# Optimization experiments

Measured on AMD Instinct MI355X. Metric: run time of the kernel, lower is better.

The kernel has to match this reference:

```python
import jax, jax.numpy as jnp
import numpy as np

H = 2048   # hidden_size
SW = 256   # stack_width
SD = 200   # stack_depth
V = 128    # input_size (vocab)
O = 128    # output_size


def setup_inputs() -> dict:
    key = jax.random.key(0)
    ks = jax.random.split(key, 14)
    s = 0.02
    return {
        'inp': jax.random.randint(ks[0], (1,), 0, V),
        'hidden': jax.random.normal(ks[1], (1, 1, H), jnp.float32),
        'stack': jax.random.normal(ks[2], (1, SD, SW), jnp.float32),
        'emb': jax.random.normal(ks[3], (V, H), jnp.float32) * s,
        'Wc': jax.random.normal(ks[4], (3, H), jnp.float32) * s,
        'bc': jax.random.normal(ks[5], (3,), jnp.float32) * s,
        'Ws': jax.random.normal(ks[6], (SW, H), jnp.float32) * s,
        'bs': jax.random.normal(ks[7], (SW,), jnp.float32) * s,
        'W_ih': jax.random.normal(ks[8], (3 * H, H + SW), jnp.float32) * s,
        'b_ih': jax.random.normal(ks[9], (3 * H,), jnp.float32) * s,
        'W_hh': jax.random.normal(ks[10], (3 * H, H), jnp.float32) * s,
        'b_hh': jax.random.normal(ks[11], (3 * H,), jnp.float32) * s,
        'Wd': jax.random.normal(ks[12], (O, H), jnp.float32) * s,
        'bd': jax.random.normal(ks[13], (O,), jnp.float32) * s,
    }


def reference(inp, hidden, stack, emb, Wc, bc, Ws, bs, W_ih, b_ih, W_hh, b_hh, Wd, bd):
    # embedding: inp.view(1,-1) -> (1,1) -> (1,1,H)
    x = emb[inp.reshape(1, -1)]
    # stack controls: softmax(Linear(hidden.squeeze(0)))  -> (1,3)
    ctrl = jax.nn.softmax(hidden[0] @ Wc.T + bc, axis=1)
    # stack input: tanh(Linear(hidden)) -> (1,1,SW); permute(1,0,2) is identity for (1,1,SW)
    s_in = jnp.tanh(hidden @ Ws.T + bs)
    s_in = jnp.transpose(s_in, (1, 0, 2))  # (batch=1, 1, SW)
    # differentiable stack push/pop/no-op
    B, _, W = stack.shape
    a_push = ctrl[:, 0][:, None, None]
    a_pop = ctrl[:, 1][:, None, None]
    a_noop = ctrl[:, 2][:, None, None]
    zeros_bot = jnp.zeros((B, 1, W), dtype=stack.dtype)
    stack_down = jnp.concatenate([stack[:, 1:], zeros_bot], axis=1)
    stack_up = jnp.concatenate([s_in, stack[:, :-1]], axis=1)
    new_stack = a_noop * stack + a_push * stack_up + a_pop * stack_down
    stack_top = new_stack[:, 0, :][None]  # (1,1,SW)
    # single-step GRU (PyTorch gate order: r, z, n)
    gin = jnp.concatenate([x, stack_top], axis=2).reshape(1, -1)  # (1, H+SW)
    h = hidden.reshape(1, -1)                                      # (1, H)
    gi = gin @ W_ih.T + b_ih
    gh = h @ W_hh.T + b_hh
    r = jax.nn.sigmoid(gi[:, :H] + gh[:, :H])
    z = jax.nn.sigmoid(gi[:, H:2 * H] + gh[:, H:2 * H])
    n = jnp.tanh(gi[:, 2 * H:] + r * gh[:, 2 * H:])
    h_new = (1.0 - z) * n + z * h
    out = h_new @ Wd.T + bd  # (1, O)
    return out, h_new[None], new_stack
```

## Files before the change

kernel.cpp:

```cpp
#include <hip/hip_runtime.h>
#include <math.h>

#define H   2048
#define SW  256
#define SD  200
#define GIN (H + SW)
#define G3H (3 * H)
#define OO  128

#define STOP_OFF 8
#define GI_OFF   512
#define GH_OFF   (GI_OFF + G3H)

__device__ __forceinline__ float wave_reduce(float v) {
#pragma unroll
    for (int off = 32; off > 0; off >>= 1)
        v += __shfl_down(v, off, 64);
    return v;
}

__device__ __forceinline__ float sigmoidf(float x) {
    return 1.f / (1.f + expf(-x));
}

__device__ __forceinline__ float dot4(float4 a, float4 b) {
    return a.x * b.x + a.y * b.y + a.z * b.z + a.w * b.w;
}

__global__ __launch_bounds__(256) void k_stack(
        const float* __restrict__ hidden,
        const float* __restrict__ stack,
        const float* __restrict__ Wc,
        const float* __restrict__ bc,
        const float* __restrict__ Ws,
        const float* __restrict__ bs,
        float* __restrict__ ws,
        float* __restrict__ out_stack ) {
    __shared__ float sc[3];
    int tid = threadIdx.x;
    if (tid < 64) {
        float c0 = 0.f, c1 = 0.f, c2 = 0.f;
        for (int k = tid; k < H; k += 64) {
            float hv = hidden[k];
            c0 += hv * Wc[k];
            c1 += hv * Wc[H + k];
            c2 += hv * Wc[2 * H + k];
        }
        c0 = wave_reduce(c0); c1 = wave_reduce(c1); c2 = wave_reduce(c2);
        if (tid == 0) {
            c0 += bc[0]; c1 += bc[1]; c2 += bc[2];
            float m = fmaxf(c0, fmaxf(c1, c2));
            float e0 = expf(c0 - m), e1 = expf(c1 - m), e2 = expf(c2 - m);
            float inv = 1.f / (e0 + e1 + e2);
            sc[0] = e0 * inv;
            sc[1] = e1 * inv;
            sc[2] = e2 * inv;
        }
    }
    __syncthreads();
    float a_push = sc[0], a_pop = sc[1], a_noop = sc[2];
    int b = blockIdx.x;
    if (b < 64) {
        int wave = tid >> 6, lane = tid & 63;
        int row = b * 4 + wave;
        const float4* h4 = (const float4*)hidden;
        const float4* w4 = (const float4*)(Ws + row * H);
        float sum = 0.f;
#pragma unroll
        for (int i = 0; i < 8; ++i) {
            float4 a = h4[lane + i * 64];
            float4 c = w4[lane + i * 64];
            sum += dot4(a, c);
        }
        sum = wave_reduce(sum);
        if (lane == 0) {
            float s = tanhf(sum + bs[row]);
            float top = a_noop * stack[row] + a_push * s + a_pop * stack[SW + row];
            ws[STOP_OFF + row] = top;
            out_stack[row] = top;
        }
    } else {
        int rbase = 1 + (b - 64) * 4;
#pragma unroll
        for (int r = 0; r < 4; ++r) {
            int row = rbase + r;
            if (row >= SD) break;
            int idx = row * SW + tid;
            float dn = (row < SD - 1) ? stack[idx + SW] : 0.f;
            out_stack[idx] = a_noop * stack[idx] + a_push * stack[idx - SW] + a_pop * dn;
        }
    }
}

__global__ __launch_bounds__(256) void k_gemv(
        const float* __restrict__ hidden,
        const float* __restrict__ emb,
        const int* __restrict__ inp,
        const float* __restrict__ W_ih, const float* __restrict__ b_ih,
        const float* __restrict__ W_hh, const float* __restrict__ b_hh,
        float* __restrict__ ws) {
    __shared__ __align__(16) float vec[GIN];
    int b = blockIdx.x;
    int tid = threadIdx.x;
    bool is_gi = (b < 384);
    if (is_gi) {
        int e = inp[0];
        const float* er = emb + (long)e * H;
        for (int k = tid; k < H; k += 256) vec[k] = er[k];
        for (int k = H + tid; k < GIN; k += 256) vec[k] = ws[STOP_OFF + (k - H)];
    } else {
        for (int k = tid; k < H; k += 256) vec[k] = hidden[k];
    }
    __syncthreads();
    int wave = tid >> 6, lane = tid & 63;
    int rbase = (is_gi ? b : b - 384) * 16 + wave * 4;
    const float* W    = is_gi ? W_ih : W_hh;
    const float* bias = is_gi ? b_ih : b_hh;
    int K  = is_gi ? GIN : H;
    int K4 = K >> 2;
    const float4* v4 = (const float4*)vec;
    const float4* w0 = (const float4*)(W + (long)(rbase + 0) * K);
    const float4* w1 = (const float4*)(W + (long)(rbase + 1) * K);
    const float4* w2 = (const float4*)(W + (long)(rbase + 2) * K);
    const float4* w3 = (const float4*)(W + (long)(rbase + 3) * K);
    float s0 = 0.f, s1 = 0.f, s2 = 0.f, s3 = 0.f;
    int i = lane;
    for (; i + 64 < K4; i += 128) {
        int j = i + 64;
        float4 a0  = v4[i],  a1  = v4[j];
        float4 b00 = w0[i],  b01 = w0[j];
        float4 b10 = w1[i],  b11 = w1[j];
        float4 b20 = w2[i],  b21 = w2[j];
        float4 b30 = w3[i],  b31 = w3[j];
        s0 += dot4(a0, b00) + dot4(a1, b01);
        s1 += dot4(a0, b10) + dot4(a1, b11);
        s2 += dot4(a0, b20) + dot4(a1, b21);
        s3 += dot4(a0, b30) + dot4(a1, b31);
    }
    if (i < K4) {
        float4 a0 = v4[i];
        s0 += dot4(a0, w0[i]);
        s1 += dot4(a0, w1[i]);
        s2 += dot4(a0, w2[i]);
        s3 += dot4(a0, w3[i]);
    }
    s0 = wave_reduce(s0);
    s1 = wave_reduce(s1);
    s2 = wave_reduce(s2);
    s3 = wave_reduce(s3);
    float* dst = ws + (is_gi ? GI_OFF : GH_OFF);
    if (lane == 0) {
        dst[rbase + 0] = s0 + bias[rbase + 0];
        dst[rbase + 1] = s1 + bias[rbase + 1];
        dst[rbase + 2] = s2 + bias[rbase + 2];
        dst[rbase + 3] = s3 + bias[rbase + 3];
    }
}

__global__ __launch_bounds__(256) void k_out(
        const float* __restrict__ hidden,
        const float* __restrict__ Wd, const float* __restrict__ bd,
        const float* __restrict__ ws,
        float* __restrict__ d_out) {
    __shared__ __align__(16) float hn[H];
    int tid = threadIdx.x;
    const float* gi = ws + GI_OFF;
    const float* gh = ws + GH_OFF;
    for (int i = tid; i < H; i += 256) {
        float r = sigmoidf(gi[i] + gh[i]);
        float z = sigmoidf(gi[H + i] + gh[H + i]);
        float n = tanhf(gi[2 * H + i] + r * gh[2 * H + i]);
        float v = (1.f - z) * n + z * hidden[i];
        hn[i] = v;
        if (blockIdx.x == 0) d_out[OO + i] = v;
    }
    __syncthreads();
    int wave = tid >> 6, lane = tid & 63;
    int row = blockIdx.x * 4 + wave;
    const float4* h4 = (const float4*)hn;
    const float4* w4 = (const float4*)(Wd + (long)row * H);
    float sum = 0.f;
#pragma unroll
    for (int i = 0; i < 8; ++i) {
        float4 a = h4[lane + i * 64];
        float4 c = w4[lane + i * 64];
        sum += dot4(a, c);
    }
    sum = wave_reduce(sum);
    if (lane == 0) d_out[row] = sum + bd[row];
}

extern "C" void kernel_launch(void* const* d_in, const int* in_sizes, int n_in,
                              void* d_out, int out_size, void* d_ws, size_t ws_size,
                              hipStream_t stream) {
    const int*   inp    = (const int*)d_in[0];
    const float* hidden = (const float*)d_in[1];
    const float* stack  = (const float*)d_in[2];
    const float* emb    = (const float*)d_in[3];
    const float* Wc     = (const float*)d_in[4];
    const float* bc     = (const float*)d_in[5];
    const float* Ws     = (const float*)d_in[6];
    const float* bs     = (const float*)d_in[7];
    const float* W_ih   = (const float*)d_in[8];
    const float* b_ih   = (const float*)d_in[9];
    const float* W_hh   = (const float*)d_in[10];
    const float* b_hh   = (const float*)d_in[11];
    const float* Wd     = (const float*)d_in[12];
    const float* bd     = (const float*)d_in[13];
    float* out = (float*)d_out;
    float* ws  = (float*)d_ws;

    k_stack<<<114, 256, 0, stream>>>(hidden, stack, Wc, bc, Ws, bs, ws, out + OO + H);
    k_gemv<<<768, 256, 0, stream>>>(hidden, emb, inp, W_ih, b_ih, W_hh, b_hh, ws);
    k_out<<<32, 256, 0, stream>>>(hidden, Wd, bd, ws, out);
}
```

Before: 179.6 us.

## Fuse three kernels into one with atomic-counter inter-block dependencies

Replaces the three sequential launches (stack update, GI/GH GEMVs, GRU+output) with one fused kernel whose blocks wait on global atomic counters. GI blocks compute the embedding portion of their dot product before spinning on the stack-top counter, which overlaps the bulk of the W_ih read with the stack computation. Output blocks spin until all GEMV blocks have signalled. This removes launch gaps and kernel boundaries, at the cost of an extra memset launch and a deadlock risk if the spinning blocks become resident before the producer blocks they wait on.

Result: slower. 330.6 us (+84.1%).

```diff
diff --git a/kernel.cpp b/kernel.cpp
--- a/kernel.cpp
+++ b/kernel.cpp
@@ -12,6 +12,17 @@
 #define GI_OFF   512
 #define GH_OFF   (GI_OFF + G3H)
 
+#define NB_SIN  64
+#define NB_ELEM 50
+#define NB_GH   384
+#define NB_GI   384
+#define NB_OUT  32
+#define B_ELEM  NB_SIN
+#define B_GH    (B_ELEM + NB_ELEM)
+#define B_GI    (B_GH + NB_GH)
+#define B_OUT   (B_GI + NB_GI)
+#define NBLK    (B_OUT + NB_OUT)
+
 __device__ __forceinline__ float wave_reduce(float v) {
 #pragma unroll
     for (int off = 32; off > 0; off >>= 1)
@@ -27,167 +38,178 @@
     return a.x * b.x + a.y * b.y + a.z * b.z + a.w * b.w;
 }
 
-__global__ __launch_bounds__(256) void k_stack(
+__device__ __forceinline__ unsigned ld_acq(const unsigned* p) {
+    return __hip_atomic_load(p, __ATOMIC_ACQUIRE, __HIP_MEMORY_SCOPE_AGENT);
+}
+
+__device__ __forceinline__ void signal_done(unsigned* c) {
+    __threadfence();
+    __hip_atomic_fetch_add(c, 1u, __ATOMIC_RELEASE, __HIP_MEMORY_SCOPE_AGENT);
+}
+
+__global__ __launch_bounds__(256, 4) void k_fused(
         const float* __restrict__ hidden,
         const float* __restrict__ stack,
-        const float* __restrict__ Wc,
-        const float* __restrict__ bc,
-        const float* __restrict__ Ws,
-        const float* __restrict__ bs,
-        float* __restrict__ ws,
-        float* __restrict__ out_stack ) {
-    __shared__ float sc[3];
-    int tid = threadIdx.x;
-    if (tid < 64) {
-        float c0 = 0.f, c1 = 0.f, c2 = 0.f;
-        for (int k = tid; k < H; k += 64) {
-            float hv = hidden[k];
-            c0 += hv * Wc[k];
-            c1 += hv * Wc[H + k];
-            c2 += hv * Wc[2 * H + k];
-        }
-        c0 = wave_reduce(c0); c1 = wave_reduce(c1); c2 = wave_reduce(c2);
-        if (tid == 0) {
-            c0 += bc[0]; c1 += bc[1]; c2 += bc[2];
-            float m = fmaxf(c0, fmaxf(c1, c2));
-            float e0 = expf(c0 - m), e1 = expf(c1 - m), e2 = expf(c2 - m);
-            float inv = 1.f / (e0 + e1 + e2);
-            sc[0] = e0 * inv;
-            sc[1] = e1 * inv;
-            sc[2] = e2 * inv;
-        }
-    }
-    __syncthreads();
-    float a_push = sc[0], a_pop = sc[1], a_noop = sc[2];
-    int b = blockIdx.x;
-    if (b < 64) {
-        int wave = tid >> 6, lane = tid & 63;
-        int row = b * 4 + wave;
-        const float4* h4 = (const float4*)hidden;
-        const float4* w4 = (const float4*)(Ws + row * H);
-        float sum = 0.f;
-#pragma unroll
-        for (int i = 0; i < 8; ++i) {
-            float4 a = h4[lane + i * 64];
-            float4 c = w4[lane + i * 64];
-            sum += dot4(a, c);
-        }
-        sum = wave_reduce(sum);
-        if (lane == 0) {
-            float s = tanhf(sum + bs[row]);
-            float top = a_noop * stack[row] + a_push * s + a_pop * stack[SW + row];
-            ws[STOP_OFF + row] = top;
-            out_stack[row] = top;
-        }
-    } else {
-        int rbase = 1 + (b - 64) * 4;
-#pragma unroll
-        for (int r = 0; r < 4; ++r) {
-            int row = rbase + r;
-            if (row >= SD) break;
-            int idx = row * SW + tid;
-            float dn = (row < SD - 1) ? stack[idx + SW] : 0.f;
-            out_stack[idx] = a_noop * stack[idx] + a_push * stack[idx - SW] + a_pop * dn;
-        }
-    }
-}
-
-__global__ __launch_bounds__(256) void k_gemv(
-        const float* __restrict__ hidden,
         const float* __restrict__ emb,
-        const int* __restrict__ inp,
+        const int*   __restrict__ inp,
+        const float* __restrict__ Wc, const float* __restrict__ bc,
+        const float* __restrict__ Ws, const float* __restrict__ bs,
         const float* __restrict__ W_ih, const float* __restrict__ b_ih,
         const float* __restrict__ W_hh, const float* __restrict__ b_hh,
-        float* __restrict__ ws) {
-    __shared__ __align__(16) float vec[GIN];
+        const float* __restrict__ Wd, const float* __restrict__ bd,
+        float* __restrict__ ws,
+        float* __restrict__ d_out) {
+    __shared__ __align__(16) float lds[H];
+    unsigned* ctr = (unsigned*)ws;
+    float* out_stack = d_out + OO + H;
     int b = blockIdx.x;
     int tid = threadIdx.x;
-    bool is_gi = (b < 384);
-    if (is_gi) {
-        int e = inp[0];
-        const float* er = emb + (long)e * H;
-        for (int k = tid; k < H; k += 256) vec[k] = er[k];
-        for (int k = H + tid; k < GIN; k += 256) vec[k] = ws[STOP_OFF + (k - H)];
-    } else {
-        for (int k = tid; k < H; k += 256) vec[k] = hidden[k];
+    int wave = tid >> 6, lane = tid & 63;
+
+    if (b < B_GH) {
+        if (tid < 64) {
+            float c0 = 0.f, c1 = 0.f, c2 = 0.f;
+            for (int k = tid; k < H; k += 64) {
+                float hv = hidden[k];
+                c0 += hv * Wc[k];
+                c1 += hv * Wc[H + k];
+                c2 += hv * Wc[2 * H + k];
+            }
+            c0 = wave_reduce(c0); c1 = wave_reduce(c1); c2 = wave_reduce(c2);
+            if (tid == 0) {
+                c0 += bc[0]; c1 += bc[1]; c2 += bc[2];
+                float m = fmaxf(c0, fmaxf(c1, c2));
+                float e0 = expf(c0 - m), e1 = expf(c1 - m), e2 = expf(c2 - m);
+                float inv = 1.f / (e0 + e1 + e2);
+                lds[0] = e0 * inv;
+                lds[1] = e1 * inv;
+                lds[2] = e2 * inv;
+            }
+        }
+        __syncthreads();
+        float a_push = lds[0], a_pop = lds[1], a_noop = lds[2];
+        if (b < B_ELEM) {
+            int row = b * 4 + wave;
+            const float4* h4 = (const float4*)hidden;
+            const float4* w4 = (const float4*)(Ws + row * H);
+            float sum = 0.f;
+#pragma unroll
+            for (int i = 0; i < 8; ++i)
+                sum += dot4(h4[lane + i * 64], w4[lane + i * 64]);
+            sum = wave_reduce(sum);
+            if (lane == 0) {
+                float s = tanhf(sum + bs[row]);
+                float top = a_noop * stack[row] + a_push * s + a_pop * stack[SW + row];
+                ws[STOP_OFF + row] = top;
+                out_stack[row] = top;
+            }
+            __syncthreads();
+            if (tid == 0) signal_done(&ctr[0]);
+        } else {
+            int rbase = 1 + (b - B_ELEM) * 4;
+#pragma unroll
+            for (int r = 0; r < 4; ++r) {
+                int row = rbase + r;
+                if (row >= SD) break;
+                int idx = row * SW + tid;
+                float dn = (row < SD - 1) ? stack[idx + SW] : 0.f;
+                out_stack[idx] = a_noop * stack[idx] + a_push * stack[idx - SW] + a_pop * dn;
+            }
+        }
+        return;
     }
-    __syncthreads();
-    int wave = tid >> 6, lane = tid & 63;
-    int rbase = (is_gi ? b : b - 384) * 16 + wave * 4;
-    const float* W    = is_gi ? W_ih : W_hh;
-    const float* bias = is_gi ? b_ih : b_hh;
-    int K  = is_gi ? GIN : H;
-    int K4 = K >> 2;
-    const float4* v4 = (const float4*)vec;
-    const float4* w0 = (const float4*)(W + (long)(rbase + 0) * K);
-    const float4* w1 = (const float4*)(W + (long)(rbase + 1) * K);
-    const float4* w2 = (const float4*)(W + (long)(rbase + 2) * K);
-    const float4* w3 = (const float4*)(W + (long)(rbase + 3) * K);
-    float s0 = 0.f, s1 = 0.f, s2 = 0.f, s3 = 0.f;
-    int i = lane;
-    for (; i + 64 < K4; i += 128) {
-        int j = i + 64;
-        float4 a0  = v4[i],  a1  = v4[j];
-        float4 b00 = w0[i],  b01 = w0[j];
-        float4 b10 = w1[i],  b11 = w1[j];
-        float4 b20 = w2[i],  b21 = w2[j];
-        float4 b30 = w3[i],  b31 = w3[j];
-        s0 += dot4(a0, b00) + dot4(a1, b01);
-        s1 += dot4(a0, b10) + dot4(a1, b11);
-        s2 += dot4(a0, b20) + dot4(a1, b21);
-        s3 += dot4(a0, b30) + dot4(a1, b31);
+
+    if (b < B_OUT) {
+        bool is_gh = (b < B_GI);
+        int idx = is_gh ? (b - B_GH) : (b - B_GI);
+        const float* srcv = is_gh ? hidden : (emb + (long)inp[0] * H);
+        {
+            float4* l4 = (float4*)lds;
+            const float4* s4 = (const float4*)srcv;
+            l4[tid] = s4[tid];
+            l4[tid + 256] = s4[tid + 256];
+        }
+        __syncthreads();
+        int K = is_gh ? H : GIN;
+        int rbase = idx * 16 + wave * 4;
+        const float* W    = is_gh ? W_hh : W_ih;
+        const float* bias = is_gh ? b_hh : b_ih;
+        const float4* v4 = (const float4*)lds;
+        const float4* w0 = (const float4*)(W + (long)(rbase + 0) * K);
+        const float4* w1 = (const float4*)(W + (long)(rbase + 1) * K);
+        const float4* w2 = (const float4*)(W + (long)(rbase + 2) * K);
+        const float4* w3 = (const float4*)(W + (long)(rbase + 3) * K);
+        float s0 = 0.f, s1 = 0.f, s2 = 0.f, s3 = 0.f;
+#pragma unroll
+        for (int u = 0; u < 4; ++u) {
+            int i = lane + u * 128, j = i + 64;
+            float4 a0 = v4[i], a1 = v4[j];
+            float4 b00 = w0[i], b01 = w0[j];
+            float4 b10 = w1[i], b11 = w1[j];
+            float4 b20 = w2[i], b21 = w2[j];
+            float4 b30 = w3[i], b31 = w3[j];
+            s0 += dot4(a0, b00) + dot4(a1, b01);
+            s1 += dot4(a0, b10) + dot4(a1, b11);
+            s2 += dot4(a0, b20) + dot4(a1, b21);
+            s3 += dot4(a0, b30) + dot4(a1, b31);
+        }
+        if (!is_gh) {
+            if (tid == 0) {
+                while (ld_acq(&ctr[0]) != (unsigned)NB_SIN) __builtin_amdgcn_s_sleep(2);
+                __threadfence();
+            }
+            __syncthreads();
+            const float4* st4 = (const float4*)(ws + STOP_OFF);
+            float4 a = st4[lane];
+            s0 += dot4(a, w0[512 + lane]);
+            s1 += dot4(a, w1[512 + lane]);
+            s2 += dot4(a, w2[512 + lane]);
+            s3 += dot4(a, w3[512 + lane]);
+        }
+        s0 = wave_reduce(s0);
+        s1 = wave_reduce(s1);
+        s2 = wave_reduce(s2);
+        s3 = wave_reduce(s3);
+        float* dst = ws + (is_gh ? GH_OFF : GI_OFF);
+        if (lane == 0) {
+            dst[rbase + 0] = s0 + bias[rbase + 0];
+            dst[rbase + 1] = s1 + bias[rbase + 1];
+            dst[rbase + 2] = s2 + bias[rbase + 2];
+            dst[rbase + 3] = s3 + bias[rbase + 3];
+        }
+        __syncthreads();
+        if (tid == 0) signal_done(&ctr[1]);
+        return;
     }
-    if (i < K4) {
-        float4 a0 = v4[i];
-        s0 += dot4(a0, w0[i]);
-        s1 += dot4(a0, w1[i]);
-        s2 += dot4(a0, w2[i]);
-        s3 += dot4(a0, w3[i]);
+
+    {
+        int idx = b - B_OUT;
+        if (tid == 0) {
+            while (ld_acq(&ctr[1]) != (unsigned)(NB_GH + NB_GI)) __builtin_amdgcn_s_sleep(2);
+            __threadfence();
+        }
+        __syncthreads();
+        const float* gi = ws + GI_OFF;
+        const float* gh = ws + GH_OFF;
+        for (int i = tid; i < H; i += 256) {
+            float r = sigmoidf(gi[i] + gh[i]);
+            float z = sigmoidf(gi[H + i] + gh[H + i]);
+            float n = tanhf(gi[2 * H + i] + r * gh[2 * H + i]);
+            float v = (1.f - z) * n + z * hidden[i];
+            lds[i] = v;
+            if (idx == 0) d_out[OO + i] = v;
+        }
+        __syncthreads();
+        int row = idx * 4 + wave;
+        const float4* h4 = (const float4*)lds;
+        const float4* w4 = (const float4*)(Wd + (long)row * H);
+        float sum = 0.f;
+#pragma unroll
+        for (int i = 0; i < 8; ++i)
+            sum += dot4(h4[lane + i * 64], w4[lane + i * 64]);
+        sum = wave_reduce(sum);
+        if (lane == 0) d_out[row] = sum + bd[row];
     }
-    s0 = wave_reduce(s0);
-    s1 = wave_reduce(s1);
-    s2 = wave_reduce(s2);
-    s3 = wave_reduce(s3);
-    float* dst = ws + (is_gi ? GI_OFF : GH_OFF);
-    if (lane == 0) {
-        dst[rbase + 0] = s0 + bias[rbase + 0];
-        dst[rbase + 1] = s1 + bias[rbase + 1];
-        dst[rbase + 2] = s2 + bias[rbase + 2];
-        dst[rbase + 3] = s3 + bias[rbase + 3];
-    }
-}
-
-__global__ __launch_bounds__(256) void k_out(
-        const float* __restrict__ hidden,
-        const float* __restrict__ Wd, const float* __restrict__ bd,
-        const float* __restrict__ ws,
-        float* __restrict__ d_out) {
-    __shared__ __align__(16) float hn[H];
-    int tid = threadIdx.x;
-    const float* gi = ws + GI_OFF;
-    const float* gh = ws + GH_OFF;
-    for (int i = tid; i < H; i += 256) {
-        float r = sigmoidf(gi[i] + gh[i]);
-        float z = sigmoidf(gi[H + i] + gh[H + i]);
-        float n = tanhf(gi[2 * H + i] + r * gh[2 * H + i]);
-        float v = (1.f - z) * n + z * hidden[i];
-        hn[i] = v;
-        if (blockIdx.x == 0) d_out[OO + i] = v;
-    }
-    __syncthreads();
-    int wave = tid >> 6, lane = tid & 63;
-    int row = blockIdx.x * 4 + wave;
-    const float4* h4 = (const float4*)hn;
-    const float4* w4 = (const float4*)(Wd + (long)row * H);
-    float sum = 0.f;
-#pragma unroll
-    for (int i = 0; i < 8; ++i) {
-        float4 a = h4[lane + i * 64];
-        float4 c = w4[lane + i * 64];
-        sum += dot4(a, c);
-    }
-    sum = wave_reduce(sum);
-    if (lane == 0) d_out[row] = sum + bd[row];
 }
 
 extern "C" void kernel_launch(void* const* d_in, const int* in_sizes, int n_in,
@@ -210,7 +232,7 @@
     float* out = (float*)d_out;
     float* ws  = (float*)d_ws;
 
-    k_stack<<<114, 256, 0, stream>>>(hidden, stack, Wc, bc, Ws, bs, ws, out + OO + H);
-    k_gemv<<<768, 256, 0, stream>>>(hidden, emb, inp, W_ih, b_ih, W_hh, b_hh, ws);
-    k_out<<<32, 256, 0, stream>>>(hidden, Wd, bd, ws, out);
-}
+    hipMemsetAsync(ws, 0, 32, stream);
+    k_fused<<<NBLK, 256, 0, stream>>>(hidden, stack, emb, inp, Wc, bc, Ws, bs,
+                                      W_ih, b_ih, W_hh, b_hh, Wd, bd, ws, out);
+}
```
